# Performance work log

Hardware: AMD Instinct MI355X
Metric: run time of the kernel (lower is better)

The kernel has to match this reference:

```python
import jax, jax.numpy as jnp
import numpy as np

NUM_EMB = 4096
EMB_DIM = 256
COMMIT = 0.25


def setup_inputs() -> dict:
    key = jax.random.key(0)
    k1, k2 = jax.random.split(key)
    z = jax.random.normal(k1, (64, 32, 32, EMB_DIM), dtype=jnp.float32)
    # torch init: uniform(-1/K, 1/K)
    codebook = jax.random.uniform(k2, (NUM_EMB, EMB_DIM), dtype=jnp.float32,
                                  minval=-1.0 / NUM_EMB, maxval=1.0 / NUM_EMB)
    return {"z": z, "codebook": codebook}


def reference(z, codebook):
    zf = z.reshape(-1, EMB_DIM)                       # [N, D]
    # ||z||^2 - 2 z.e + ||e||^2  -> [N, K]
    d = (jnp.sum(zf * zf, axis=1, keepdims=True)
         - 2.0 * (zf @ codebook.T)
         + jnp.sum(codebook * codebook, axis=1))
    idx = jnp.argmin(d, axis=1)                       # [N]
    z_q = codebook[idx].reshape(z.shape)              # gather replaces one-hot matmul
    sg = jax.lax.stop_gradient
    loss = jnp.mean((sg(z_q) - z) ** 2) + COMMIT * jnp.mean((z_q - sg(z)) ** 2)
    z_q_ste = z + sg(z_q - z)                         # straight-through
    return z_q_ste, loss
```

## Files before the change

kernel.cpp:

```cpp
#include <hip/hip_runtime.h>
#include <hip/hip_bf16.h>
#include <stdint.h>

#define NUM_EMB 4096
#define EMB_DIM 256
#define NVEC 65536
#define OUT0_SIZE (NVEC * EMB_DIM)
#define MTILE 128
#define NTILE 64
#define LROW 528
#define DCONST 0.0625f

typedef __bf16 bf16x8 __attribute__((ext_vector_type(8)));
typedef float floatx16 __attribute__((ext_vector_type(16)));

static __device__ __forceinline__ unsigned int f2bf(float f) {
  unsigned int u = __float_as_uint(f);
  return (u + 0x7fffu + ((u >> 16) & 1u)) >> 16;
}

static __device__ __forceinline__ uint4 pack_bf8(float4 a, float4 b) {
  uint4 r;
  r.x = f2bf(a.x) | (f2bf(a.y) << 16);
  r.y = f2bf(a.z) | (f2bf(a.w) << 16);
  r.z = f2bf(b.x) | (f2bf(b.y) << 16);
  r.w = f2bf(b.z) | (f2bf(b.w) << 16);
  return r;
}

__global__ void __launch_bounds__(256) vq_prep(const float* __restrict__ cbf,
                                               unsigned short* __restrict__ cbb,
                                               float* __restrict__ enorm,
                                               float* __restrict__ out) {
  int w = threadIdx.x >> 6;
  int lane = threadIdx.x & 63;
  int row = blockIdx.x * 4 + w;
  float4 v = ((const float4*)(cbf + (size_t)row * EMB_DIM))[lane];
  float ss = v.x * v.x + v.y * v.y + v.z * v.z + v.w * v.w;
  ushort4 b;
  b.x = (unsigned short)f2bf(v.x);
  b.y = (unsigned short)f2bf(v.y);
  b.z = (unsigned short)f2bf(v.z);
  b.w = (unsigned short)f2bf(v.w);
  ((ushort4*)(cbb + (size_t)row * EMB_DIM))[lane] = b;
#pragma unroll
  for (int m = 1; m < 64; m <<= 1) ss += __shfl_xor(ss, m, 64);
  if (lane == 0) enorm[row] = ss + DCONST;
  if (blockIdx.x == 0 && threadIdx.x == 0) out[OUT0_SIZE] = 0.0f;
}

__global__ void __launch_bounds__(256, 2) vq_main(const float* __restrict__ z,
                                                  const float* __restrict__ cbf,
                                                  const unsigned short* __restrict__ cbb,
                                                  const float* __restrict__ enorm,
                                                  float* __restrict__ out) {
  __shared__ unsigned char stage[NTILE * LROW];
  __shared__ float lds_en[NTILE];
  __shared__ unsigned int minlds[2][MTILE];
  __shared__ float znorm[MTILE];
  __shared__ int idx_lds[MTILE];
  __shared__ float wsum[4];

  const int t = threadIdx.x;
  const int w = t >> 6;
  const int lane = t & 63;
  const int h = lane >> 5;
  const int eL = lane & 31;
  const int rg = w & 1;
  const int cg = w >> 1;
  const int blk = blockIdx.x;
  const int row_base = blk * MTILE + rg * 64;

  uint4 afrag[2][16];
  float zn[2] = {0.f, 0.f};
#pragma unroll
  for (int g = 0; g < 2; ++g) {
    const float* rp = z + (size_t)(row_base + g * 32 + eL) * EMB_DIM + h * 8;
#pragma unroll
    for (int ks = 0; ks < 16; ++ks) {
      float4 a0 = *(const float4*)(rp + ks * 16);
      float4 a1 = *(const float4*)(rp + ks * 16 + 4);
      zn[g] += a0.x * a0.x + a0.y * a0.y + a0.z * a0.z + a0.w * a0.w
             + a1.x * a1.x + a1.y * a1.y + a1.z * a1.z + a1.w * a1.w;
      afrag[g][ks] = pack_bf8(a0, a1);
    }
    zn[g] += __shfl_xor(zn[g], 32, 64);
  }
  if (w < 2 && h == 0) {
    znorm[rg * 64 + eL] = zn[0];
    znorm[rg * 64 + 32 + eL] = zn[1];
  }

  unsigned int pmin[32];
#pragma unroll
  for (int s = 0; s < 32; ++s) pmin[s] = 0xFFFFFFFFu;

  for (int c0 = 0; c0 < NUM_EMB; c0 += NTILE) {
    __syncthreads();
#pragma unroll
    for (int j = 0; j < 8; ++j) {
      int id = t + 256 * j;
      int e = id >> 5, kc = id & 31;
      uint4 v = *(const uint4*)(cbb + (size_t)(c0 + e) * EMB_DIM + kc * 8);
      *(uint4*)(stage + e * LROW + kc * 16) = v;
    }
    if (t < NTILE) lds_en[t] = enorm[c0 + t];
    __syncthreads();

    floatx16 acc0, acc1;
#pragma unroll
    for (int r = 0; r < 16; ++r) { acc0[r] = 0.f; acc1[r] = 0.f; }
    const unsigned char* bp = stage + (cg * 32 + eL) * LROW + h * 16;
#pragma unroll
    for (int ks = 0; ks < 16; ++ks) {
      bf16x8 b = __builtin_bit_cast(bf16x8, *(const uint4*)(bp + ks * 32));
      acc0 = __builtin_amdgcn_mfma_f32_32x32x16_bf16(
          __builtin_bit_cast(bf16x8, afrag[0][ks]), b, acc0, 0, 0, 0);
      acc1 = __builtin_amdgcn_mfma_f32_32x32x16_bf16(
          __builtin_bit_cast(bf16x8, afrag[1][ks]), b, acc1, 0, 0, 0);
    }

    float enC = lds_en[cg * 32 + eL];
    unsigned int colb = (unsigned int)(c0 + cg * 32 + eL);
#pragma unroll
    for (int reg = 0; reg < 16; ++reg) {
      float d0 = fmaf(-2.f, acc0[reg], enC);
      unsigned int p0 = (__float_as_uint(d0) & 0xFFFFF000u) | colb;
      if (p0 < pmin[reg]) pmin[reg] = p0;
      float d1 = fmaf(-2.f, acc1[reg], enC);
      unsigned int p1 = (__float_as_uint(d1) & 0xFFFFF000u) | colb;
      if (p1 < pmin[16 + reg]) pmin[16 + reg] = p1;
    }
  }

#pragma unroll
  for (int s = 0; s < 32; ++s) {
    unsigned int v = pmin[s];
#pragma unroll
    for (int m = 1; m <= 16; m <<= 1) {
      unsigned int o = __shfl_xor(v, m, 64);
      if (o < v) v = o;
    }
    pmin[s] = v;
  }
  if (eL == 0) {
#pragma unroll
    for (int s = 0; s < 32; ++s) {
      int g = s >> 4, reg = s & 15;
      int rowl = rg * 64 + g * 32 + (reg & 3) + 8 * (reg >> 2) + 4 * h;
      minlds[cg][rowl] = pmin[s];
    }
  }
  __syncthreads();

  float rl = 0.f;
  if (t < MTILE) {
    unsigned int m0 = minlds[0][t], m1 = minlds[1][t];
    unsigned int m = m1 < m0 ? m1 : m0;
    idx_lds[t] = (int)(m & 0xFFFu);
    rl = znorm[t] + __uint_as_float(m & 0xFFFFF000u) - DCONST;
  }
#pragma unroll
  for (int m = 1; m < 64; m <<= 1) rl += __shfl_xor(rl, m, 64);
  if (lane == 0) wsum[w] = rl;
  __syncthreads();
  if (t == 0) {
    float s = (wsum[0] + wsum[1]) + (wsum[2] + wsum[3]);
    atomicAdd(out + OUT0_SIZE, s * (1.25f / (float)OUT0_SIZE));
  }

#pragma unroll 4
  for (int j = 0; j < 32; ++j) {
    int id4 = j * 256 + t;
    int r = id4 >> 6, c4 = id4 & 63;
    int k = idx_lds[r];
    float4 ev = ((const float4*)(cbf + (size_t)k * EMB_DIM))[c4];
    ((float4*)(out + (size_t)(blk * MTILE + r) * EMB_DIM))[c4] = ev;
  }
}

extern "C" void kernel_launch(void* const* d_in, const int* in_sizes, int n_in,
                              void* d_out, int out_size, void* d_ws, size_t ws_size,
                              hipStream_t stream) {
  const float* z = (const float*)d_in[0];
  const float* cbf = (const float*)d_in[1];
  unsigned short* cbb = (unsigned short*)d_ws;
  float* enorm = (float*)((char*)d_ws + (size_t)NUM_EMB * EMB_DIM * 2);
  float* out = (float*)d_out;
  vq_prep<<<NUM_EMB / 4, 256, 0, stream>>>(cbf, cbb, enorm, out);
  vq_main<<<NVEC / MTILE, 256, 0, stream>>>(z, cbf, cbb, enorm, out);
}
```

Baseline: 264.7 us.

## Double-buffer codebook tiles with async global-to-LDS loads and XOR swizzle

Replaces the register-staged, padded codebook tile copy with a double-buffered LDS stage filled by global_load_lds direct loads. The next tile's load is issued before computing the current one, and one barrier per iteration replaces two. An XOR swizzle replaces row padding to avoid bank conflicts. The per-row z norm is now reduced per wave and folded into the loss sum. This doubles LDS use, which may limit occupancy, and it depends on how the async load completes relative to the barrier.

```diff
diff --git a/kernel.cpp b/kernel.cpp
--- a/kernel.cpp
+++ b/kernel.cpp
@@ -8,7 +8,6 @@
 #define OUT0_SIZE (NVEC * EMB_DIM)
 #define MTILE 128
 #define NTILE 64
-#define LROW 528
 #define DCONST 0.0625f
 
 typedef __bf16 bf16x8 __attribute__((ext_vector_type(8)));
@@ -54,12 +53,11 @@
                                                   const unsigned short* __restrict__ cbb,
                                                   const float* __restrict__ enorm,
                                                   float* __restrict__ out) {
-  __shared__ unsigned char stage[NTILE * LROW];
-  __shared__ float lds_en[NTILE];
+  __shared__ __align__(16) unsigned char sstage[2][NTILE * 512];
   __shared__ unsigned int minlds[2][MTILE];
-  __shared__ float znorm[MTILE];
   __shared__ int idx_lds[MTILE];
   __shared__ float wsum[4];
+  __shared__ float zwsum[2];
 
   const int t = threadIdx.x;
   const int w = t >> 6;
@@ -71,6 +69,22 @@
   const int blk = blockIdx.x;
   const int row_base = blk * MTILE + rg * 64;
 
+  auto stage_tile = [&](int buf, int c0) {
+#pragma unroll
+    for (int j = 0; j < 8; ++j) {
+      int e = (w << 4) + (j << 1) + h;
+      int s = eL ^ (e & 7);
+      const unsigned short* src = cbb + ((size_t)(c0 + e) << 8) + (s << 3);
+      __builtin_amdgcn_global_load_lds(
+          (const __attribute__((address_space(1))) void*)src,
+          (__attribute__((address_space(3))) void*)&sstage[buf][(w << 13) + (j << 10)],
+          16, 0, 0);
+    }
+  };
+
+  stage_tile(0, 0);
+  float enC = enorm[cg * 32 + eL];
+
   uint4 afrag[2][16];
   float zn[2] = {0.f, 0.f};
 #pragma unroll
@@ -86,41 +100,43 @@
     }
     zn[g] += __shfl_xor(zn[g], 32, 64);
   }
-  if (w < 2 && h == 0) {
-    znorm[rg * 64 + eL] = zn[0];
-    znorm[rg * 64 + 32 + eL] = zn[1];
+  if (cg == 0) {
+    float zs = zn[0] + zn[1];
+#pragma unroll
+    for (int m = 1; m <= 16; m <<= 1) zs += __shfl_xor(zs, m, 64);
+    if (lane == 0) zwsum[rg] = zs;
   }
 
   unsigned int pmin[32];
 #pragma unroll
   for (int s = 0; s < 32; ++s) pmin[s] = 0xFFFFFFFFu;
 
+  __syncthreads();
+
+  const int sx4 = (eL & 7) << 4;
+  int cur = 0;
   for (int c0 = 0; c0 < NUM_EMB; c0 += NTILE) {
-    __syncthreads();
-#pragma unroll
-    for (int j = 0; j < 8; ++j) {
-      int id = t + 256 * j;
-      int e = id >> 5, kc = id & 31;
-      uint4 v = *(const uint4*)(cbb + (size_t)(c0 + e) * EMB_DIM + kc * 8);
-      *(uint4*)(stage + e * LROW + kc * 16) = v;
-    }
-    if (t < NTILE) lds_en[t] = enorm[c0 + t];
-    __syncthreads();
+    int c1 = c0 + NTILE;
+    float enN = enC;
+    if (c1 < NUM_EMB) {
+      stage_tile(cur ^ 1, c1);
+      enN = enorm[c1 + cg * 32 + eL];
+    }
 
     floatx16 acc0, acc1;
 #pragma unroll
     for (int r = 0; r < 16; ++r) { acc0[r] = 0.f; acc1[r] = 0.f; }
-    const unsigned char* bp = stage + (cg * 32 + eL) * LROW + h * 16;
+    const unsigned char* bp = &sstage[cur][(cg * 32 + eL) * 512];
 #pragma unroll
     for (int ks = 0; ks < 16; ++ks) {
-      bf16x8 b = __builtin_bit_cast(bf16x8, *(const uint4*)(bp + ks * 32));
+      uint4 bv = *(const uint4*)(bp + ((ks * 32 + h * 16) ^ sx4));
+      bf16x8 b = __builtin_bit_cast(bf16x8, bv);
       acc0 = __builtin_amdgcn_mfma_f32_32x32x16_bf16(
           __builtin_bit_cast(bf16x8, afrag[0][ks]), b, acc0, 0, 0, 0);
       acc1 = __builtin_amdgcn_mfma_f32_32x32x16_bf16(
           __builtin_bit_cast(bf16x8, afrag[1][ks]), b, acc1, 0, 0, 0);
     }
 
-    float enC = lds_en[cg * 32 + eL];
     unsigned int colb = (unsigned int)(c0 + cg * 32 + eL);
 #pragma unroll
     for (int reg = 0; reg < 16; ++reg) {
@@ -131,6 +147,10 @@
       unsigned int p1 = (__float_as_uint(d1) & 0xFFFFF000u) | colb;
       if (p1 < pmin[16 + reg]) pmin[16 + reg] = p1;
     }
+
+    __syncthreads();
+    cur ^= 1;
+    enC = enN;
   }
 
 #pragma unroll
@@ -158,14 +178,14 @@
     unsigned int m0 = minlds[0][t], m1 = minlds[1][t];
     unsigned int m = m1 < m0 ? m1 : m0;
     idx_lds[t] = (int)(m & 0xFFFu);
-    rl = znorm[t] + __uint_as_float(m & 0xFFFFF000u) - DCONST;
+    rl = __uint_as_float(m & 0xFFFFF000u) - DCONST;
   }
 #pragma unroll
   for (int m = 1; m < 64; m <<= 1) rl += __shfl_xor(rl, m, 64);
   if (lane == 0) wsum[w] = rl;
   __syncthreads();
   if (t == 0) {
-    float s = (wsum[0] + wsum[1]) + (wsum[2] + wsum[3]);
+    float s = (wsum[0] + wsum[1]) + (wsum[2] + wsum[3]) + zwsum[0] + zwsum[1];
     atomicAdd(out + OUT0_SIZE, s * (1.25f / (float)OUT0_SIZE));
   }
 
```

Result: no change. 261.7 us (-1.1%).

## Load codebook B-fragments directly from global memory instead of LDS staging

Applied to the files above, without the earlier changes.

The main loop no longer stages each 64-entry bf16 codebook tile into shared memory behind two barriers. Each lane now reads its MFMA B operand and its codebook norm straight from global memory, relying on L1/L2 caching because every block rereads the same 2 MB codebook. This removes the per-tile __syncthreads and LDS traffic, but uses uncoalesced 16-byte reads with a stride of one codebook row across lanes, and latency is no longer hidden by cooperative staging. The per-row z-norm buffer is replaced by a wave-level partial sum folded into the final loss reduction, and the running min uses min() instead of a branch.

```diff
diff --git a/kernel.cpp b/kernel.cpp
--- a/kernel.cpp
+++ b/kernel.cpp
@@ -8,7 +8,6 @@
 #define OUT0_SIZE (NVEC * EMB_DIM)
 #define MTILE 128
 #define NTILE 64
-#define LROW 528
 #define DCONST 0.0625f
 
 typedef __bf16 bf16x8 __attribute__((ext_vector_type(8)));
@@ -54,12 +53,10 @@
                                                   const unsigned short* __restrict__ cbb,
                                                   const float* __restrict__ enorm,
                                                   float* __restrict__ out) {
-  __shared__ unsigned char stage[NTILE * LROW];
-  __shared__ float lds_en[NTILE];
   __shared__ unsigned int minlds[2][MTILE];
-  __shared__ float znorm[MTILE];
   __shared__ int idx_lds[MTILE];
   __shared__ float wsum[4];
+  __shared__ float zwsum[2];
 
   const int t = threadIdx.x;
   const int w = t >> 6;
@@ -86,50 +83,45 @@
     }
     zn[g] += __shfl_xor(zn[g], 32, 64);
   }
-  if (w < 2 && h == 0) {
-    znorm[rg * 64 + eL] = zn[0];
-    znorm[rg * 64 + 32 + eL] = zn[1];
+  if (cg == 0) {
+    float zs = zn[0] + zn[1];
+#pragma unroll
+    for (int m = 1; m <= 16; m <<= 1) zs += __shfl_xor(zs, m, 64);
+    if (lane == 0) zwsum[rg] = zs;
   }
 
   unsigned int pmin[32];
 #pragma unroll
   for (int s = 0; s < 32; ++s) pmin[s] = 0xFFFFFFFFu;
 
+  const int col = cg * 32 + eL;
+  const uint4* bbase = (const uint4*)cbb + (size_t)col * 32 + h;
+
   for (int c0 = 0; c0 < NUM_EMB; c0 += NTILE) {
-    __syncthreads();
-#pragma unroll
-    for (int j = 0; j < 8; ++j) {
-      int id = t + 256 * j;
-      int e = id >> 5, kc = id & 31;
-      uint4 v = *(const uint4*)(cbb + (size_t)(c0 + e) * EMB_DIM + kc * 8);
-      *(uint4*)(stage + e * LROW + kc * 16) = v;
-    }
-    if (t < NTILE) lds_en[t] = enorm[c0 + t];
-    __syncthreads();
+    float enC = enorm[c0 + col];
+    const uint4* bq = bbase + (size_t)c0 * 32;
 
     floatx16 acc0, acc1;
 #pragma unroll
     for (int r = 0; r < 16; ++r) { acc0[r] = 0.f; acc1[r] = 0.f; }
-    const unsigned char* bp = stage + (cg * 32 + eL) * LROW + h * 16;
 #pragma unroll
     for (int ks = 0; ks < 16; ++ks) {
-      bf16x8 b = __builtin_bit_cast(bf16x8, *(const uint4*)(bp + ks * 32));
+      bf16x8 b = __builtin_bit_cast(bf16x8, bq[ks * 2]);
       acc0 = __builtin_amdgcn_mfma_f32_32x32x16_bf16(
           __builtin_bit_cast(bf16x8, afrag[0][ks]), b, acc0, 0, 0, 0);
       acc1 = __builtin_amdgcn_mfma_f32_32x32x16_bf16(
           __builtin_bit_cast(bf16x8, afrag[1][ks]), b, acc1, 0, 0, 0);
     }
 
-    float enC = lds_en[cg * 32 + eL];
-    unsigned int colb = (unsigned int)(c0 + cg * 32 + eL);
+    unsigned int colb = (unsigned int)(c0 + col);
 #pragma unroll
     for (int reg = 0; reg < 16; ++reg) {
       float d0 = fmaf(-2.f, acc0[reg], enC);
       unsigned int p0 = (__float_as_uint(d0) & 0xFFFFF000u) | colb;
-      if (p0 < pmin[reg]) pmin[reg] = p0;
+      pmin[reg] = min(pmin[reg], p0);
       float d1 = fmaf(-2.f, acc1[reg], enC);
       unsigned int p1 = (__float_as_uint(d1) & 0xFFFFF000u) | colb;
-      if (p1 < pmin[16 + reg]) pmin[16 + reg] = p1;
+      pmin[16 + reg] = min(pmin[16 + reg], p1);
     }
   }
 
@@ -158,14 +150,14 @@
     unsigned int m0 = minlds[0][t], m1 = minlds[1][t];
     unsigned int m = m1 < m0 ? m1 : m0;
     idx_lds[t] = (int)(m & 0xFFFu);
-    rl = znorm[t] + __uint_as_float(m & 0xFFFFF000u) - DCONST;
+    rl = __uint_as_float(m & 0xFFFFF000u) - DCONST;
   }
 #pragma unroll
   for (int m = 1; m < 64; m <<= 1) rl += __shfl_xor(rl, m, 64);
   if (lane == 0) wsum[w] = rl;
   __syncthreads();
   if (t == 0) {
-    float s = (wsum[0] + wsum[1]) + (wsum[2] + wsum[3]);
+    float s = (wsum[0] + wsum[1]) + (wsum[2] + wsum[3]) + zwsum[0] + zwsum[1];
     atomicAdd(out + OUT0_SIZE, s * (1.25f / (float)OUT0_SIZE));
   }
 
```

Measured after the change: 365.8 us. 1.38x slower.
